# Performance work log

Measured on AMD Instinct MI355X. Metric: run time of the kernel, lower is better.

Reference implementation:

```python
import jax, jax.numpy as jnp
import numpy as np

V, C, D, L, H = 32000, 1024, 1024, 12, 16
HD = D // H


def setup_inputs() -> dict:
    key = jax.random.key(0)
    ks = jax.random.split(key, 20)
    B, T = 2, 1024
    s = 0.02
    inp = {
        "context": jax.random.randint(ks[0], (B, T), 0, V),
        "tok_emb": jax.random.normal(ks[1], (V, D), jnp.float32) * s,
        "pos_emb": jax.random.normal(ks[2], (C, D), jnp.float32) * s,
        # per-layer stacked params (weights stored [in, out])
        "wq": jax.random.normal(ks[3], (L, D, D), jnp.float32) * s,
        "wk": jax.random.normal(ks[4], (L, D, D), jnp.float32) * s,
        "wv": jax.random.normal(ks[5], (L, D, D), jnp.float32) * s,
        "ln1_s": jnp.ones((L, D), jnp.float32),
        "ln1_b": jnp.zeros((L, D), jnp.float32),
        "ln2_s": jnp.ones((L, D), jnp.float32),
        "ln2_b": jnp.zeros((L, D), jnp.float32),
        "fw1": jax.random.normal(ks[6], (L, D, D), jnp.float32) * s,
        "fb1": jnp.zeros((L, D), jnp.float32),
        "fw2": jax.random.normal(ks[7], (L, D, D), jnp.float32) * s,
        "fb2": jnp.zeros((L, D), jnp.float32),
        "lnf_s": jnp.ones((D,), jnp.float32),
        "lnf_b": jnp.zeros((D,), jnp.float32),
        "wp": jax.random.normal(ks[8], (D, V), jnp.float32) * s,
        "bp": jnp.zeros((V,), jnp.float32),
    }
    return inp


def _ln(x, scale, bias, eps=1e-5):
    m = jnp.mean(x, axis=-1, keepdims=True)
    v = jnp.mean(jnp.square(x - m), axis=-1, keepdims=True)
    return (x - m) * jax.lax.rsqrt(v + eps) * scale + bias


def reference(context, tok_emb, pos_emb, wq, wk, wv, ln1_s, ln1_b, ln2_s, ln2_b,
              fw1, fb1, fw2, fb2, lnf_s, lnf_b, wp, bp):
    B, T = context.shape
    x = tok_emb[context] + pos_emb[:T]  # [B,T,D]
    causal = jnp.tril(jnp.ones((T, T), bool))

    def block(x, p):
        (wq_, wk_, wv_, s1, b1, s2, b2, w1_, b1f, w2_, b2f) = p
        h = _ln(x, s1, b1)
        # concatenated per-head projections == full [D,D] matmul + head reshape
        q = (h @ wq_).reshape(B, T, H, HD)
        k = (h @ wk_).reshape(B, T, H, HD)
        v = (h @ wv_).reshape(B, T, H, HD)
        scores = jnp.einsum('bthd,bshd->bhts', q, k) / np.sqrt(HD)
        scores = jnp.where(causal, scores, -jnp.inf)
        attn = jax.nn.softmax(scores, axis=-1)
        o = jnp.einsum('bhts,bshd->bthd', attn, v).reshape(B, T, D)
        x = x + o
        h2 = _ln(x, s2, b2)
        f = jax.nn.relu(h2 @ w1_ + b1f) @ w2_ + b2f  # dropout in eval mode (identity)
        return x + f, None

    x, _ = jax.lax.scan(block, x, (wq, wk, wv, ln1_s, ln1_b, ln2_s, ln2_b, fw1, fb1, fw2, fb2))
    logits = _ln(x, lnf_s, lnf_b) @ wp + bp
    return jax.nn.softmax(logits, axis=-1)
```

## Files before the change

### kernel.cpp

```cpp
#include <hip/hip_runtime.h>
#include <hip/hip_bf16.h>

typedef unsigned short u16;
typedef float f32x4 __attribute__((ext_vector_type(4)));
typedef __bf16 bf16x8 __attribute__((ext_vector_type(8)));
typedef short s16x8 __attribute__((ext_vector_type(8)));


__device__ __forceinline__ u16 f2b(float f) {
  union { __hip_bfloat16 h; u16 u; } c;
  c.h = __float2bfloat16(f);
  return c.u;
}

__device__ __forceinline__ void gload16(const void* g, void* l) {
  __builtin_amdgcn_global_load_lds(
      (const __attribute__((address_space(1))) unsigned int*)g,
      (__attribute__((address_space(3))) unsigned int*)l, 16, 0, 0);
}

__device__ __forceinline__ float block_sum(float v, float* sred) {
  const int tid = threadIdx.x;
#pragma unroll
  for (int off = 32; off >= 1; off >>= 1) v += __shfl_down(v, off);
  if ((tid & 63) == 0) sred[tid >> 6] = v;
  __syncthreads();
  float r = sred[0] + sred[1] + sred[2] + sred[3];
  __syncthreads();
  return r;
}

__device__ __forceinline__ f32x4 fmax4(f32x4 a, f32x4 b) {
  f32x4 r;
  r[0] = fmaxf(a[0], b[0]); r[1] = fmaxf(a[1], b[1]);
  r[2] = fmaxf(a[2], b[2]); r[3] = fmaxf(a[3], b[3]);
  return r;
}


template<int ROWS>
__device__ __forceinline__ void stage_tile(const u16* g, int ld, char* ldsb, int tid) {
#pragma unroll
  for (int i = 0; i < ROWS / 64; ++i) {
    int c = i * 256 + tid;
    int row = c >> 2;
    int k8 = (c & 3) ^ ((row >> 1) & 3);
    gload16(g + (size_t)row * ld + k8 * 8, ldsb + i * 4096 + (tid & 192) * 16);
  }
}

template<int MI, int NI, int WCN>
__device__ __forceinline__ void compute_tile(const char* lA, const char* lB, f32x4 (&acc)[MI][NI]) {
  const int tid = threadIdx.x;
  const int lane = tid & 63;
  const int w = tid >> 6;
  const int wr = w / WCN, wc = w % WCN;
  const int fr = lane & 15, k8 = lane >> 4;
  bf16x8 a[MI], b[NI];
#pragma unroll
  for (int mi = 0; mi < MI; ++mi) {
    int row = wr * (MI * 16) + mi * 16 + fr;
    a[mi] = *(const bf16x8*)(lA + row * 64 + ((k8 ^ ((row >> 1) & 3)) << 4));
  }
#pragma unroll
  for (int ni = 0; ni < NI; ++ni) {
    int row = wc * (NI * 16) + ni * 16 + fr;
    b[ni] = *(const bf16x8*)(lB + row * 64 + ((k8 ^ ((row >> 1) & 3)) << 4));
  }
#pragma unroll
  for (int mi = 0; mi < MI; ++mi)
#pragma unroll
    for (int ni = 0; ni < NI; ++ni)
      acc[mi][ni] = __builtin_amdgcn_mfma_f32_16x16x32_bf16(a[mi], b[ni], acc[mi][ni], 0, 0, 0);
}

template<int MI, int NI, int WRN, int WCN, int BMT, int BNT>
__device__ __forceinline__ void gemm_core(const u16* A, int lda, const u16* B, int ldb,
                                          int nkt, char* lds, f32x4 (&acc)[MI][NI]) {
  const int tid = threadIdx.x;
  const int bufSz = BMT * 64 + BNT * 64;
  stage_tile<BMT>(A, lda, lds, tid);
  stage_tile<BNT>(B, ldb, lds + BMT * 64, tid);
  __syncthreads();
  int cur = 0;
  for (int kt = 0; kt < nkt; ++kt) {
    if (kt + 1 < nkt) {
      char* nb = lds + (cur ^ 1) * bufSz;
      stage_tile<BMT>(A + (size_t)(kt + 1) * 32, lda, nb, tid);
      stage_tile<BNT>(B + (size_t)(kt + 1) * 32, ldb, nb + BMT * 64, tid);
    }
    char* cb = lds + cur * bufSz;
    compute_tile<MI, NI, WCN>(cb, cb + BMT * 64, acc);
    __syncthreads();
    cur ^= 1;
  }
}


template<int ROWS>
__device__ __forceinline__ void stage64(const u16* g, int ld, char* ldsb, int tid) {
#pragma unroll
  for (int i = 0; i < ROWS / 32; ++i) {
    int c = i * 256 + tid;
    int row = c >> 3;
    int slot = (c & 7) ^ (row & 7);
    gload16(g + (size_t)row * ld + slot * 8, ldsb + i * 4096 + (tid & 192) * 16);
  }
}

__device__ __forceinline__ bf16x8 ldread64(const char* base, int row, int slot) {
  return *(const bf16x8*)(base + row * 128 + ((slot ^ (row & 7)) << 4));
}


__global__ __launch_bounds__(256) void embed_kernel(const int* __restrict__ ctx,
    const float* __restrict__ tok, const float* __restrict__ pos, float* __restrict__ x) {
  const int row = blockIdx.x, tid = threadIdx.x;
  const int t = row & 1023;
  const int id = ctx[row];
  float4 a = ((const float4*)(tok + (size_t)id * 1024))[tid];
  float4 p = ((const float4*)(pos + (size_t)t * 1024))[tid];
  a.x += p.x; a.y += p.y; a.z += p.z; a.w += p.w;
  ((float4*)(x + (size_t)row * 1024))[tid] = a;
}

__global__ __launch_bounds__(256) void layernorm_bf16(const float* __restrict__ x,
    const float* __restrict__ sc, const float* __restrict__ bi, u16* __restrict__ h) {
  __shared__ float sred[4];
  const int row = blockIdx.x, tid = threadIdx.x;
  const float4 v = ((const float4*)(x + (size_t)row * 1024))[tid];
  float mean = block_sum(v.x + v.y + v.z + v.w, sred) * (1.f / 1024.f);
  const float dx = v.x - mean, dy = v.y - mean, dz = v.z - mean, dw = v.w - mean;
  float var = block_sum(dx * dx + dy * dy + dz * dz + dw * dw, sred) * (1.f / 1024.f);
  const float rs = rsqrtf(var + 1e-5f);
  const float4 s4 = ((const float4*)sc)[tid];
  const float4 b4 = ((const float4*)bi)[tid];
  ushort4 o;
  o.x = f2b(dx * rs * s4.x + b4.x);
  o.y = f2b(dy * rs * s4.y + b4.y);
  o.z = f2b(dz * rs * s4.z + b4.z);
  o.w = f2b(dw * rs * s4.w + b4.w);
  ((ushort4*)(h + (size_t)row * 1024))[tid] = o;
}

__device__ __forceinline__ void transpose_body(const float* __restrict__ src,
                                               u16* __restrict__ dst, int N) {
  __shared__ float tile[32][33];
  const int tid = threadIdx.x;
  const int tx = tid & 31, ty = tid >> 5;
  const int kt = blockIdx.y * 32, nt = blockIdx.x * 32;
#pragma unroll
  for (int i = 0; i < 4; ++i) {
    int r = ty + i * 8;
    tile[r][tx] = src[(size_t)(kt + r) * N + nt + tx];
  }
  __syncthreads();
#pragma unroll
  for (int i = 0; i < 4; ++i) {
    int r = ty + i * 8;
    dst[(size_t)(nt + r) * 1024 + kt + tx] = f2b(tile[tx][r]);
  }
}

__global__ __launch_bounds__(256) void transpose_cvt(const float* __restrict__ src,
    u16* __restrict__ dst, int N, size_t srcStride, size_t dstStride) {
  transpose_body(src + blockIdx.z * srcStride, dst + blockIdx.z * dstStride, N);
}

__global__ __launch_bounds__(256) void transpose_qkv(const float* __restrict__ wq,
    const float* __restrict__ wk, const float* __restrict__ wv, u16* __restrict__ dst) {
  const int z = blockIdx.z, l = z / 3, which = z - l * 3;
  const float* src = (which == 0 ? wq : (which == 1 ? wk : wv)) + (size_t)l * 1048576;
  u16* d = dst + (size_t)l * 3145728 + (size_t)which * 1048576;
  transpose_body(src, d, 1024);
}

template<int MI, int NI, int WRN, int WCN, bool BIAS, bool RELU, bool RESID, bool OUTBF, bool XSWAP>
__global__ __launch_bounds__(256) void gemm_bt(const u16* __restrict__ A, int lda,
    const u16* __restrict__ Bt, int ldb, const float* __restrict__ bias,
    const float* __restrict__ resid, void* __restrict__ out, int ldc, int nkt) {
  constexpr int BMT = WRN * MI * 16;
  constexpr int BNT = WCN * NI * 16;
  __shared__ __align__(128) char lds[2 * (BMT * 64 + BNT * 64)];
  const int bmi = XSWAP ? blockIdx.x : blockIdx.y;
  const int bni = XSWAP ? blockIdx.y : blockIdx.x;
  const size_t bm = (size_t)bmi * BMT, bn = (size_t)bni * BNT;
  const f32x4 vz = {0.f, 0.f, 0.f, 0.f};
  f32x4 acc[MI][NI];
#pragma unroll
  for (int i = 0; i < MI; ++i)
#pragma unroll
    for (int j = 0; j < NI; ++j) acc[i][j] = vz;
  gemm_core<MI, NI, WRN, WCN, BMT, BNT>(A + bm * lda, lda, Bt + bn * ldb, ldb, nkt, lds, acc);
  const int tid = threadIdx.x, lane = tid & 63, w = tid >> 6;
  const int wr = w / WCN, wc = w % WCN, fr = lane & 15, k8 = lane >> 4;
#pragma unroll
  for (int mi = 0; mi < MI; ++mi)
#pragma unroll
    for (int ni = 0; ni < NI; ++ni) {
      const size_t c = bn + wc * (NI * 16) + ni * 16 + fr;
      const float bv = BIAS ? bias[c] : 0.f;
#pragma unroll
      for (int j = 0; j < 4; ++j) {
        const size_t r = bm + wr * (MI * 16) + mi * 16 + k8 * 4 + j;
        float v = acc[mi][ni][j] + bv;
        if (RELU) v = fmaxf(v, 0.f);
        if (RESID) v += resid[r * (size_t)ldc + c];
        if (OUTBF) ((u16*)out)[r * (size_t)ldc + c] = f2b(v);
        else       ((float*)out)[r * (size_t)ldc + c] = v;
      }
    }
}

__global__ __launch_bounds__(256) void gather_vT(const u16* __restrict__ qkv,
    u16* __restrict__ vT) {
  const int st = blockIdx.x;
  const int bh = blockIdx.y;
  const int b = bh >> 4, h = bh & 15;
  __shared__ u16 tile[64][80];
  const int tid = threadIdx.x;
#pragma unroll
  for (int i = 0; i < 2; ++i) {
    int c = i * 256 + tid;
    int sl = c >> 3, h8 = c & 7;
    *(s16x8*)&tile[sl][h8 * 8] =
        *(const s16x8*)(qkv + (size_t)(b * 1024 + st * 64 + sl) * 3072 + 2048 + h * 64 + h8 * 8);
  }
  __syncthreads();
#pragma unroll
  for (int i = 0; i < 2; ++i) {
    int c = i * 256 + tid;
    int hd = c >> 3, s8 = c & 7;
    s16x8 o;
#pragma unroll
    for (int j = 0; j < 8; ++j) o[j] = (short)tile[s8 * 8 + j][hd];
    *(s16x8*)(vT + ((size_t)bh * 64 + hd) * 1024 + st * 64 + s8 * 8) = o;
  }
}

__global__ __launch_bounds__(256) void attn_flash(const u16* __restrict__ qkv,
    const u16* __restrict__ vT, float* __restrict__ x) {
  const int tt = blockIdx.x;
  const int bh = blockIdx.y;
  const int b = bh >> 4, h = bh & 15;
  __shared__ __align__(128) char lds[65536];
  char* Qs = lds;
  char* Ks = lds + 16384;
  char* Vs = lds + 32768;
  const int tid = threadIdx.x, lane = tid & 63, w = tid >> 6;
  const int fr = lane & 15, k8 = lane >> 4;
  char* Pw = lds + 49152 + w * 4096;
  const u16* qbase = qkv + (size_t)(b * 1024 + tt * 128) * 3072 + h * 64;
  const u16* kbase = qkv + (size_t)(b * 1024) * 3072 + 1024 + h * 64;
  const u16* vbase = vT + (size_t)bh * 65536;

  stage64<128>(qbase, 3072, Qs, tid);
  stage64<64>(kbase, 3072, Ks, tid);
  stage64<64>(vbase, 1024, Vs, tid);
  __syncthreads();

  bf16x8 aq[2][2];
#pragma unroll
  for (int mi = 0; mi < 2; ++mi)
#pragma unroll
    for (int kk = 0; kk < 2; ++kk)
      aq[mi][kk] = ldread64(Qs, w * 32 + mi * 16 + fr, kk * 4 + k8);

  const f32x4 vz = {0.f, 0.f, 0.f, 0.f};
  const f32x4 vninf = {-1e30f, -1e30f, -1e30f, -1e30f};
  f32x4 oacc[2][4], m_[2], l_[2];
#pragma unroll
  for (int mi = 0; mi < 2; ++mi) {
    m_[mi] = vninf; l_[mi] = vz;
#pragma unroll
    for (int ni = 0; ni < 4; ++ni) oacc[mi][ni] = vz;
  }

  const int nst = tt * 2 + 2;
  const int t0 = tt * 128 + w * 32;
  int cur = 0;
  for (int st = 0; st < nst; ++st) {
    if (st + 1 < nst) {
      stage64<64>(kbase + (size_t)(st + 1) * 64 * 3072, 3072, Ks + (cur ^ 1) * 8192, tid);
      stage64<64>(vbase + (st + 1) * 64, 1024, Vs + (cur ^ 1) * 8192, tid);
    }
    if (st * 64 <= t0 + 31) {
      const char* Kc = Ks + cur * 8192;
      const char* Vc = Vs + cur * 8192;
      f32x4 sacc[2][4];
#pragma unroll
      for (int mi = 0; mi < 2; ++mi)
#pragma unroll
        for (int ni = 0; ni < 4; ++ni) sacc[mi][ni] = vz;
#pragma unroll
      for (int kk = 0; kk < 2; ++kk) {
        bf16x8 bk[4];
#pragma unroll
        for (int ni = 0; ni < 4; ++ni) bk[ni] = ldread64(Kc, ni * 16 + fr, kk * 4 + k8);
#pragma unroll
        for (int mi = 0; mi < 2; ++mi)
#pragma unroll
          for (int ni = 0; ni < 4; ++ni)
            sacc[mi][ni] = __builtin_amdgcn_mfma_f32_16x16x32_bf16(aq[mi][kk], bk[ni], sacc[mi][ni], 0, 0, 0);
      }
      const int sbase = st * 64;
      const bool needMask = (sbase + 63 > t0);
#pragma unroll
      for (int mi = 0; mi < 2; ++mi) {
#pragma unroll
        for (int ni = 0; ni < 4; ++ni) {
          sacc[mi][ni] *= 0.125f;
          if (needMask) {
            const int s = sbase + ni * 16 + fr;
#pragma unroll
            for (int j = 0; j < 4; ++j) {
              const int t = t0 + mi * 16 + k8 * 4 + j;
              if (s > t) sacc[mi][ni][j] = -1e30f;
            }
          }
        }
        f32x4 pm = fmax4(fmax4(sacc[mi][0], sacc[mi][1]), fmax4(sacc[mi][2], sacc[mi][3]));
#pragma unroll
        for (int msk = 1; msk <= 8; msk <<= 1) {
#pragma unroll
          for (int j = 0; j < 4; ++j) pm[j] = fmaxf(pm[j], __shfl_xor(pm[j], msk));
        }
        const f32x4 mn = fmax4(m_[mi], pm);
        f32x4 alpha, rs = vz;
#pragma unroll
        for (int j = 0; j < 4; ++j) alpha[j] = __expf(m_[mi][j] - mn[j]);
#pragma unroll
        for (int ni = 0; ni < 4; ++ni) {
#pragma unroll
          for (int j = 0; j < 4; ++j) {
            const float p = __expf(sacc[mi][ni][j] - mn[j]);
            rs[j] += p;
            const int t_loc = mi * 16 + k8 * 4 + j;
            const int s_loc = ni * 16 + fr;
            *(u16*)(Pw + t_loc * 128 + (((s_loc >> 3) ^ (t_loc & 7)) << 4) + (s_loc & 7) * 2) = f2b(p);
          }
        }
#pragma unroll
        for (int msk = 1; msk <= 8; msk <<= 1) {
#pragma unroll
          for (int j = 0; j < 4; ++j) rs[j] += __shfl_xor(rs[j], msk);
        }
        m_[mi] = mn;
#pragma unroll
        for (int j = 0; j < 4; ++j) l_[mi][j] = l_[mi][j] * alpha[j] + rs[j];
#pragma unroll
        for (int ni = 0; ni < 4; ++ni) oacc[mi][ni] *= alpha;
      }
#pragma unroll
      for (int kk = 0; kk < 2; ++kk) {
        bf16x8 ap[2], bv[4];
#pragma unroll
        for (int mi = 0; mi < 2; ++mi) ap[mi] = ldread64(Pw, mi * 16 + fr, kk * 4 + k8);
#pragma unroll
        for (int ni = 0; ni < 4; ++ni) bv[ni] = ldread64(Vc, ni * 16 + fr, kk * 4 + k8);
#pragma unroll
        for (int mi = 0; mi < 2; ++mi)
#pragma unroll
          for (int ni = 0; ni < 4; ++ni)
            oacc[mi][ni] = __builtin_amdgcn_mfma_f32_16x16x32_bf16(ap[mi], bv[ni], oacc[mi][ni], 0, 0, 0);
      }
    }
    __syncthreads();
    cur ^= 1;
  }
#pragma unroll
  for (int mi = 0; mi < 2; ++mi) {
    f32x4 invl;
#pragma unroll
    for (int j = 0; j < 4; ++j) invl[j] = 1.f / l_[mi][j];
#pragma unroll
    for (int ni = 0; ni < 4; ++ni) {
      const int hd = ni * 16 + fr;
#pragma unroll
      for (int j = 0; j < 4; ++j) {
        const int t = tt * 128 + w * 32 + mi * 16 + k8 * 4 + j;
        x[(size_t)(b * 1024 + t) * 1024 + h * 64 + hd] += oacc[mi][ni][j] * invl[j];
      }
    }
  }
}

__global__ __launch_bounds__(256) void softmax_v(float* __restrict__ logits) {
  const int row = blockIdx.x, tid = threadIdx.x;
  float* lr = logits + (size_t)row * 32000;
  const float4* lr4 = (const float4*)lr;
  float mx = -1e30f, sm = 0.f;
  for (int i = tid; i < 8000; i += 256) {
    const float4 v = lr4[i];
    float vm = fmaxf(fmaxf(v.x, v.y), fmaxf(v.z, v.w));
    float m2 = fmaxf(mx, vm);
    sm = sm * __expf(mx - m2) + __expf(v.x - m2) + __expf(v.y - m2) +
         __expf(v.z - m2) + __expf(v.w - m2);
    mx = m2;
  }
  __shared__ float smx[4], ssm[4];
#pragma unroll
  for (int off = 32; off >= 1; off >>= 1) {
    float om = __shfl_down(mx, off), os = __shfl_down(sm, off);
    float m2 = fmaxf(mx, om);
    sm = sm * __expf(mx - m2) + os * __expf(om - m2);
    mx = m2;
  }
  if ((tid & 63) == 0) { smx[tid >> 6] = mx; ssm[tid >> 6] = sm; }
  __syncthreads();
  const float M = fmaxf(fmaxf(smx[0], smx[1]), fmaxf(smx[2], smx[3]));
  const float S = ssm[0] * __expf(smx[0] - M) + ssm[1] * __expf(smx[1] - M) +
                  ssm[2] * __expf(smx[2] - M) + ssm[3] * __expf(smx[3] - M);
  const float inv = 1.f / S;
  float4* lw4 = (float4*)lr;
  for (int i = tid; i < 8000; i += 256) {
    float4 v = lw4[i];
    v.x = __expf(v.x - M) * inv; v.y = __expf(v.y - M) * inv;
    v.z = __expf(v.z - M) * inv; v.w = __expf(v.w - M) * inv;
    lw4[i] = v;
  }
}


extern "C" void kernel_launch(void* const* d_in, const int* in_sizes, int n_in,
                              void* d_out, int out_size, void* d_ws, size_t ws_size,
                              hipStream_t stream) {
  const int*   ctx   = (const int*)d_in[0];
  const float* tok   = (const float*)d_in[1];
  const float* pos   = (const float*)d_in[2];
  const float* wq    = (const float*)d_in[3];
  const float* wk    = (const float*)d_in[4];
  const float* wv    = (const float*)d_in[5];
  const float* ln1_s = (const float*)d_in[6];
  const float* ln1_b = (const float*)d_in[7];
  const float* ln2_s = (const float*)d_in[8];
  const float* ln2_b = (const float*)d_in[9];
  const float* fw1   = (const float*)d_in[10];
  const float* fb1   = (const float*)d_in[11];
  const float* fw2   = (const float*)d_in[12];
  const float* fb2   = (const float*)d_in[13];
  const float* lnf_s = (const float*)d_in[14];
  const float* lnf_b = (const float*)d_in[15];
  const float* wp    = (const float*)d_in[16];
  const float* bp    = (const float*)d_in[17];
  float* out = (float*)d_out;

  char* ws = (char*)d_ws;
  size_t o = 0;
  auto get = [&](size_t bytes) {
    char* r = ws + o;
    o += (bytes + 255) & ~(size_t)255;
    return r;
  };
  u16*   wqkvT = (u16*)get(12ULL * 3072 * 1024 * 2);
  u16*   wf1T  = (u16*)get(12ULL * 1024 * 1024 * 2);
  u16*   wf2T  = (u16*)get(12ULL * 1024 * 1024 * 2);
  u16*   wpT   = (u16*)get(32000ULL * 1024 * 2);
  float* x     = (float*)get(2048ULL * 1024 * 4);
  u16*   h     = (u16*)get(2048ULL * 1024 * 2);
  u16*   qkvb  = (u16*)get(2048ULL * 3072 * 2);
  u16*   vT    = (u16*)get(32ULL * 64 * 1024 * 2);
  u16*   f1b   = (u16*)get(2048ULL * 1024 * 2);

  embed_kernel<<<2048, 256, 0, stream>>>(ctx, tok, pos, x);
  transpose_qkv<<<dim3(32, 32, 36), 256, 0, stream>>>(wq, wk, wv, wqkvT);
  transpose_cvt<<<dim3(32, 32, 12), 256, 0, stream>>>(fw1, wf1T, 1024, 1048576, 1048576);
  transpose_cvt<<<dim3(32, 32, 12), 256, 0, stream>>>(fw2, wf2T, 1024, 1048576, 1048576);
  transpose_cvt<<<dim3(1000, 32, 1), 256, 0, stream>>>(wp, wpT, 32000, 0, 0);

  for (int l = 0; l < 12; ++l) {
    layernorm_bf16<<<2048, 256, 0, stream>>>(x, ln1_s + l * 1024, ln1_b + l * 1024, h);
    gemm_bt<4, 4, 2, 2, false, false, false, true, false><<<dim3(24, 16), 256, 0, stream>>>(
        h, 1024, wqkvT + (size_t)l * 3145728, 1024, nullptr, nullptr, qkvb, 3072, 32);
    gather_vT<<<dim3(16, 32), 256, 0, stream>>>(qkvb, vT);
    attn_flash<<<dim3(8, 32), 256, 0, stream>>>(qkvb, vT, x);
    layernorm_bf16<<<2048, 256, 0, stream>>>(x, ln2_s + l * 1024, ln2_b + l * 1024, h);
    gemm_bt<4, 2, 2, 2, true, true, false, true, false><<<dim3(16, 16), 256, 0, stream>>>(
        h, 1024, wf1T + (size_t)l * 1048576, 1024, fb1 + l * 1024, nullptr, f1b, 1024, 32);
    gemm_bt<4, 2, 2, 2, true, false, true, false, false><<<dim3(16, 16), 256, 0, stream>>>(
        f1b, 1024, wf2T + (size_t)l * 1048576, 1024, fb2 + l * 1024, x, x, 1024, 32);
  }

  layernorm_bf16<<<2048, 256, 0, stream>>>(x, lnf_s, lnf_b, h);
  gemm_bt<4, 4, 2, 2, true, false, false, false, true><<<dim3(16, 250), 256, 0, stream>>>(
      h, 1024, wpT, 1024, bp, nullptr, out, 32000, 32);
  softmax_v<<<2048, 256, 0, stream>>>(out);
}
```

Before: 2.427 ms.

## Shrink attention query tiles to 64 rows and swizzle vocab GEMM block order

```diff
diff --git a/kernel.cpp b/kernel.cpp
--- a/kernel.cpp
+++ b/kernel.cpp
@@ -175,15 +175,24 @@
   transpose_body(src, d, 1024);
 }
 
-template<int MI, int NI, int WRN, int WCN, bool BIAS, bool RELU, bool RESID, bool OUTBF, bool XSWAP>
+template<int MI, int NI, int WRN, int WCN, bool BIAS, bool RELU, bool RESID, bool OUTBF,
+         bool XSWAP, int SWIZ>
 __global__ __launch_bounds__(256) void gemm_bt(const u16* __restrict__ A, int lda,
     const u16* __restrict__ Bt, int ldb, const float* __restrict__ bias,
     const float* __restrict__ resid, void* __restrict__ out, int ldc, int nkt) {
   constexpr int BMT = WRN * MI * 16;
   constexpr int BNT = WCN * NI * 16;
   __shared__ __align__(128) char lds[2 * (BMT * 64 + BNT * 64)];
-  const int bmi = XSWAP ? blockIdx.x : blockIdx.y;
-  const int bni = XSWAP ? blockIdx.y : blockIdx.x;
+  int bmi, bni;
+  if (SWIZ > 0) {
+    const int v = blockIdx.x;
+    const int vp = (v & 7) * SWIZ + (v >> 3);
+    bni = vp >> 4;
+    bmi = vp & 15;
+  } else {
+    bmi = XSWAP ? blockIdx.x : blockIdx.y;
+    bni = XSWAP ? blockIdx.y : blockIdx.x;
+  }
   const size_t bm = (size_t)bmi * BMT, bn = (size_t)bni * BNT;
   const f32x4 vz = {0.f, 0.f, 0.f, 0.f};
   f32x4 acc[MI][NI];
@@ -240,147 +249,127 @@
 
 __global__ __launch_bounds__(256) void attn_flash(const u16* __restrict__ qkv,
     const u16* __restrict__ vT, float* __restrict__ x) {
-  const int tt = blockIdx.x;
-  const int bh = blockIdx.y;
+  const int bh = blockIdx.x;
+  const int qt = blockIdx.y;
   const int b = bh >> 4, h = bh & 15;
-  __shared__ __align__(128) char lds[65536];
+  __shared__ __align__(128) char lds[40960];
   char* Qs = lds;
-  char* Ks = lds + 16384;
-  char* Vs = lds + 32768;
+  char* Ks = lds + 8192;
+  char* Vs = lds + 24576;
   const int tid = threadIdx.x, lane = tid & 63, w = tid >> 6;
   const int fr = lane & 15, k8 = lane >> 4;
-  char* Pw = lds + 49152 + w * 4096;
-  const u16* qbase = qkv + (size_t)(b * 1024 + tt * 128) * 3072 + h * 64;
+  char* Pw = Qs + w * 2048;
+  const u16* qbase = qkv + (size_t)(b * 1024 + qt * 64) * 3072 + h * 64;
   const u16* kbase = qkv + (size_t)(b * 1024) * 3072 + 1024 + h * 64;
   const u16* vbase = vT + (size_t)bh * 65536;
 
-  stage64<128>(qbase, 3072, Qs, tid);
+  stage64<64>(qbase, 3072, Qs, tid);
   stage64<64>(kbase, 3072, Ks, tid);
   stage64<64>(vbase, 1024, Vs, tid);
   __syncthreads();
 
-  bf16x8 aq[2][2];
-#pragma unroll
-  for (int mi = 0; mi < 2; ++mi)
-#pragma unroll
-    for (int kk = 0; kk < 2; ++kk)
-      aq[mi][kk] = ldread64(Qs, w * 32 + mi * 16 + fr, kk * 4 + k8);
+  bf16x8 aq[2];
+#pragma unroll
+  for (int kk = 0; kk < 2; ++kk)
+    aq[kk] = ldread64(Qs, w * 16 + fr, kk * 4 + k8);
 
   const f32x4 vz = {0.f, 0.f, 0.f, 0.f};
-  const f32x4 vninf = {-1e30f, -1e30f, -1e30f, -1e30f};
-  f32x4 oacc[2][4], m_[2], l_[2];
-#pragma unroll
-  for (int mi = 0; mi < 2; ++mi) {
-    m_[mi] = vninf; l_[mi] = vz;
-#pragma unroll
-    for (int ni = 0; ni < 4; ++ni) oacc[mi][ni] = vz;
-  }
-
-  const int nst = tt * 2 + 2;
-  const int t0 = tt * 128 + w * 32;
+  f32x4 oacc[4];
+  f32x4 m_ = {-1e30f, -1e30f, -1e30f, -1e30f};
+  f32x4 l_ = vz;
+#pragma unroll
+  for (int ni = 0; ni < 4; ++ni) oacc[ni] = vz;
+
+  const int nst = qt + 1;
+  const int t0 = qt * 64 + w * 16;
   int cur = 0;
   for (int st = 0; st < nst; ++st) {
     if (st + 1 < nst) {
       stage64<64>(kbase + (size_t)(st + 1) * 64 * 3072, 3072, Ks + (cur ^ 1) * 8192, tid);
       stage64<64>(vbase + (st + 1) * 64, 1024, Vs + (cur ^ 1) * 8192, tid);
     }
-    if (st * 64 <= t0 + 31) {
-      const char* Kc = Ks + cur * 8192;
-      const char* Vc = Vs + cur * 8192;
-      f32x4 sacc[2][4];
-#pragma unroll
-      for (int mi = 0; mi < 2; ++mi)
-#pragma unroll
-        for (int ni = 0; ni < 4; ++ni) sacc[mi][ni] = vz;
-#pragma unroll
-      for (int kk = 0; kk < 2; ++kk) {
-        bf16x8 bk[4];
-#pragma unroll
-        for (int ni = 0; ni < 4; ++ni) bk[ni] = ldread64(Kc, ni * 16 + fr, kk * 4 + k8);
-#pragma unroll
-        for (int mi = 0; mi < 2; ++mi)
-#pragma unroll
-          for (int ni = 0; ni < 4; ++ni)
-            sacc[mi][ni] = __builtin_amdgcn_mfma_f32_16x16x32_bf16(aq[mi][kk], bk[ni], sacc[mi][ni], 0, 0, 0);
+    const char* Kc = Ks + cur * 8192;
+    const char* Vc = Vs + cur * 8192;
+    f32x4 sacc[4];
+#pragma unroll
+    for (int ni = 0; ni < 4; ++ni) sacc[ni] = vz;
+#pragma unroll
+    for (int kk = 0; kk < 2; ++kk) {
+      bf16x8 bk[4];
+#pragma unroll
+      for (int ni = 0; ni < 4; ++ni) bk[ni] = ldread64(Kc, ni * 16 + fr, kk * 4 + k8);
+#pragma unroll
+      for (int ni = 0; ni < 4; ++ni)
+        sacc[ni] = __builtin_amdgcn_mfma_f32_16x16x32_bf16(aq[kk], bk[ni], sacc[ni], 0, 0, 0);
+    }
+    const int sbase = st * 64;
+    const bool needMask = (st == qt);
+#pragma unroll
+    for (int ni = 0; ni < 4; ++ni) {
+      sacc[ni] *= 0.125f;
+      if (needMask) {
+        const int s = sbase + ni * 16 + fr;
+#pragma unroll
+        for (int j = 0; j < 4; ++j) {
+          const int t = t0 + k8 * 4 + j;
+          if (s > t) sacc[ni][j] = -1e30f;
+        }
       }
-      const int sbase = st * 64;
-      const bool needMask = (sbase + 63 > t0);
-#pragma unroll
-      for (int mi = 0; mi < 2; ++mi) {
-#pragma unroll
-        for (int ni = 0; ni < 4; ++ni) {
-          sacc[mi][ni] *= 0.125f;
-          if (needMask) {
-            const int s = sbase + ni * 16 + fr;
-#pragma unroll
-            for (int j = 0; j < 4; ++j) {
-              const int t = t0 + mi * 16 + k8 * 4 + j;
-              if (s > t) sacc[mi][ni][j] = -1e30f;
-            }
-          }
-        }
-        f32x4 pm = fmax4(fmax4(sacc[mi][0], sacc[mi][1]), fmax4(sacc[mi][2], sacc[mi][3]));
-#pragma unroll
-        for (int msk = 1; msk <= 8; msk <<= 1) {
-#pragma unroll
-          for (int j = 0; j < 4; ++j) pm[j] = fmaxf(pm[j], __shfl_xor(pm[j], msk));
-        }
-        const f32x4 mn = fmax4(m_[mi], pm);
-        f32x4 alpha, rs = vz;
-#pragma unroll
-        for (int j = 0; j < 4; ++j) alpha[j] = __expf(m_[mi][j] - mn[j]);
-#pragma unroll
-        for (int ni = 0; ni < 4; ++ni) {
-#pragma unroll
-          for (int j = 0; j < 4; ++j) {
-            const float p = __expf(sacc[mi][ni][j] - mn[j]);
-            rs[j] += p;
-            const int t_loc = mi * 16 + k8 * 4 + j;
-            const int s_loc = ni * 16 + fr;
-            *(u16*)(Pw + t_loc * 128 + (((s_loc >> 3) ^ (t_loc & 7)) << 4) + (s_loc & 7) * 2) = f2b(p);
-          }
-        }
-#pragma unroll
-        for (int msk = 1; msk <= 8; msk <<= 1) {
-#pragma unroll
-          for (int j = 0; j < 4; ++j) rs[j] += __shfl_xor(rs[j], msk);
-        }
-        m_[mi] = mn;
-#pragma unroll
-        for (int j = 0; j < 4; ++j) l_[mi][j] = l_[mi][j] * alpha[j] + rs[j];
-#pragma unroll
-        for (int ni = 0; ni < 4; ++ni) oacc[mi][ni] *= alpha;
+    }
+    f32x4 pm = fmax4(fmax4(sacc[0], sacc[1]), fmax4(sacc[2], sacc[3]));
+#pragma unroll
+    for (int msk = 1; msk <= 8; msk <<= 1) {
+#pragma unroll
+      for (int j = 0; j < 4; ++j) pm[j] = fmaxf(pm[j], __shfl_xor(pm[j], msk));
+    }
+    const f32x4 mn = fmax4(m_, pm);
+    f32x4 alpha, rs = vz;
+#pragma unroll
+    for (int j = 0; j < 4; ++j) alpha[j] = __expf(m_[j] - mn[j]);
+#pragma unroll
+    for (int ni = 0; ni < 4; ++ni) {
+#pragma unroll
+      for (int j = 0; j < 4; ++j) {
+        const float p = __expf(sacc[ni][j] - mn[j]);
+        rs[j] += p;
+        const int t_loc = k8 * 4 + j;
+        const int s_loc = ni * 16 + fr;
+        *(u16*)(Pw + t_loc * 128 + (((s_loc >> 3) ^ (t_loc & 7)) << 4) + (s_loc & 7) * 2) = f2b(p);
       }
-#pragma unroll
-      for (int kk = 0; kk < 2; ++kk) {
-        bf16x8 ap[2], bv[4];
-#pragma unroll
-        for (int mi = 0; mi < 2; ++mi) ap[mi] = ldread64(Pw, mi * 16 + fr, kk * 4 + k8);
-#pragma unroll
-        for (int ni = 0; ni < 4; ++ni) bv[ni] = ldread64(Vc, ni * 16 + fr, kk * 4 + k8);
-#pragma unroll
-        for (int mi = 0; mi < 2; ++mi)
-#pragma unroll
-          for (int ni = 0; ni < 4; ++ni)
-            oacc[mi][ni] = __builtin_amdgcn_mfma_f32_16x16x32_bf16(ap[mi], bv[ni], oacc[mi][ni], 0, 0, 0);
-      }
+    }
+#pragma unroll
+    for (int msk = 1; msk <= 8; msk <<= 1) {
+#pragma unroll
+      for (int j = 0; j < 4; ++j) rs[j] += __shfl_xor(rs[j], msk);
+    }
+    m_ = mn;
+#pragma unroll
+    for (int j = 0; j < 4; ++j) l_[j] = l_[j] * alpha[j] + rs[j];
+#pragma unroll
+    for (int ni = 0; ni < 4; ++ni) oacc[ni] *= alpha;
+#pragma unroll
+    for (int kk = 0; kk < 2; ++kk) {
+      bf16x8 ap = ldread64(Pw, fr, kk * 4 + k8);
+      bf16x8 bv[4];
+#pragma unroll
+      for (int ni = 0; ni < 4; ++ni) bv[ni] = ldread64(Vc, ni * 16 + fr, kk * 4 + k8);
+#pragma unroll
+      for (int ni = 0; ni < 4; ++ni)
+        oacc[ni] = __builtin_amdgcn_mfma_f32_16x16x32_bf16(ap, bv[ni], oacc[ni], 0, 0, 0);
     }
     __syncthreads();
     cur ^= 1;
   }
-#pragma unroll
-  for (int mi = 0; mi < 2; ++mi) {
-    f32x4 invl;
-#pragma unroll
-    for (int j = 0; j < 4; ++j) invl[j] = 1.f / l_[mi][j];
-#pragma unroll
-    for (int ni = 0; ni < 4; ++ni) {
-      const int hd = ni * 16 + fr;
-#pragma unroll
-      for (int j = 0; j < 4; ++j) {
-        const int t = tt * 128 + w * 32 + mi * 16 + k8 * 4 + j;
-        x[(size_t)(b * 1024 + t) * 1024 + h * 64 + hd] += oacc[mi][ni][j] * invl[j];
-      }
+  f32x4 invl;
+#pragma unroll
+  for (int j = 0; j < 4; ++j) invl[j] = 1.f / l_[j];
+#pragma unroll
+  for (int ni = 0; ni < 4; ++ni) {
+    const int hd = ni * 16 + fr;
+#pragma unroll
+    for (int j = 0; j < 4; ++j) {
+      const int t = t0 + k8 * 4 + j;
+      x[(size_t)(b * 1024 + t) * 1024 + h * 64 + hd] += oacc[ni][j] * invl[j];
     }
   }
 }
@@ -470,19 +459,19 @@
 
   for (int l = 0; l < 12; ++l) {
     layernorm_bf16<<<2048, 256, 0, stream>>>(x, ln1_s + l * 1024, ln1_b + l * 1024, h);
-    gemm_bt<4, 4, 2, 2, false, false, false, true, false><<<dim3(24, 16), 256, 0, stream>>>(
+    gemm_bt<4, 4, 2, 2, false, false, false, true, false, 0><<<dim3(24, 16), 256, 0, stream>>>(
         h, 1024, wqkvT + (size_t)l * 3145728, 1024, nullptr, nullptr, qkvb, 3072, 32);
     gather_vT<<<dim3(16, 32), 256, 0, stream>>>(qkvb, vT);
-    attn_flash<<<dim3(8, 32), 256, 0, stream>>>(qkvb, vT, x);
+    attn_flash<<<dim3(32, 16), 256, 0, stream>>>(qkvb, vT, x);
     layernorm_bf16<<<2048, 256, 0, stream>>>(x, ln2_s + l * 1024, ln2_b + l * 1024, h);
-    gemm_bt<4, 2, 2, 2, true, true, false, true, false><<<dim3(16, 16), 256, 0, stream>>>(
+    gemm_bt<4, 2, 2, 2, true, true, false, true, false, 0><<<dim3(16, 16), 256, 0, stream>>>(
         h, 1024, wf1T + (size_t)l * 1048576, 1024, fb1 + l * 1024, nullptr, f1b, 1024, 32);
-    gemm_bt<4, 2, 2, 2, true, false, true, false, false><<<dim3(16, 16), 256, 0, stream>>>(
+    gemm_bt<4, 2, 2, 2, true, false, true, false, false, 0><<<dim3(16, 16), 256, 0, stream>>>(
         f1b, 1024, wf2T + (size_t)l * 1048576, 1024, fb2 + l * 1024, x, x, 1024, 32);
   }
 
   layernorm_bf16<<<2048, 256, 0, stream>>>(x, lnf_s, lnf_b, h);
-  gemm_bt<4, 4, 2, 2, true, false, false, false, true><<<dim3(16, 250), 256, 0, stream>>>(
+  gemm_bt<4, 4, 2, 2, true, false, false, false, false, 500><<<dim3(4000), 256, 0, stream>>>(
       h, 1024, wpT, 1024, bp, nullptr, out, 32000, 32);
   softmax_v<<<2048, 256, 0, stream>>>(out);
 }
```

New measurement: 2.198 ms. -9.4%, faster.
